# Kernel tuning notes

Hardware: AMD Instinct MI355X
Metric: run time of the kernel (lower is better)

The kernel has to match this reference:

```python
import jax, jax.numpy as jnp
import numpy as np

N, E, DIN, H, DOUT, NBLK = 50000, 300000, 963, 256, 3, 6


def gconv(x, src, dst, ew, W, Wl, b):
    # support = x @ W ; out[i] = sum_j ew_ij * support[j] + x[i] @ W_loop + b
    sup = x @ W
    agg = jax.ops.segment_sum(ew[:, None] * sup[src], dst, num_segments=N)
    return agg + x @ Wl + b


def setup_inputs() -> dict:
    key = jax.random.key(0)
    ks = jax.random.split(key, 16)
    s = 0.05
    x = jax.random.normal(ks[0], (N, DIN), jnp.float32)
    src = jax.random.randint(ks[1], (E,), 0, N, dtype=jnp.int32)
    dst = jax.random.randint(ks[2], (E,), 0, N, dtype=jnp.int32)
    ew = jax.random.uniform(ks[3], (E,), jnp.float32)
    W1 = jax.random.normal(ks[4], (DIN, H), jnp.float32) * s
    Wl1 = jax.random.normal(ks[5], (DIN, H), jnp.float32) * s
    b1 = jnp.zeros((H,), jnp.float32)
    # stacked residual-block weights: [NBLK, 2 convs, H, H]
    blkW = jax.random.normal(ks[6], (NBLK, 2, H, H), jnp.float32) * s
    blkWl = jax.random.normal(ks[7], (NBLK, 2, H, H), jnp.float32) * s
    blkb = jnp.zeros((NBLK, 2, H), jnp.float32)
    W2 = jax.random.normal(ks[8], (H, DOUT), jnp.float32) * s
    Wl2 = jax.random.normal(ks[9], (H, DOUT), jnp.float32) * s
    b2 = jnp.zeros((DOUT,), jnp.float32)
    return dict(x=x, src=src, dst=dst, ew=ew, W1=W1, Wl1=Wl1, b1=b1,
                blkW=blkW, blkWl=blkWl, blkb=blkb, W2=W2, Wl2=Wl2, b2=b2)


def reference(x, src, dst, ew, W1, Wl1, b1, blkW, blkWl, blkb, W2, Wl2, b2):
    h = jax.nn.relu(gconv(x, src, dst, ew, W1, Wl1, b1))

    def block(h, p):
        W, Wl, b = p  # W: [2,H,H]
        y = jax.nn.relu(gconv(h, src, dst, ew, W[0], Wl[0], b[0]))
        y = jax.nn.relu(gconv(y, src, dst, ew, W[1], Wl[1], b[1]))
        return (h + y) * 0.5, None

    x_hidden, _ = jax.lax.scan(block, h, (blkW, blkWl, blkb))
    x_out = gconv(x_hidden, src, dst, ew, W2, Wl2, b2)
    return (x_out, x_hidden)
```

## Files before the change

kernel.cpp:

```cpp
#include <hip/hip_runtime.h>

typedef __attribute__((ext_vector_type(8))) short short8;
typedef __attribute__((ext_vector_type(4))) float f32x4;

constexpr int kN = 50000;
constexpr int kE = 300000;
constexpr int kDIN = 963;
constexpr int kH = 256;
constexpr int kNBLK = 6;

__device__ inline unsigned short f2bf(float f) {
    unsigned u = __float_as_uint(f);
    u = u + 0x7FFFu + ((u >> 16) & 1u);
    return (unsigned short)(u >> 16);
}
__device__ inline float bf2f(unsigned short s) {
    return __uint_as_float(((unsigned)s) << 16);
}

__device__ inline void gload_lds16(const void* g, void* l) {
    __builtin_amdgcn_global_load_lds(
        (const __attribute__((address_space(1))) void*)g,
        (__attribute__((address_space(3))) void*)l, 16, 0, 0);
}

__global__ __launch_bounds__(512) void gemm_l1(
    const float* __restrict__ Av, const unsigned short* __restrict__ Bt,
    const float* __restrict__ bias,
    unsigned short* __restrict__ supb, unsigned short* __restrict__ tpreb,
    int M, int Kpad, int Kvalid, int Astride)
{
    __shared__ __align__(16) char smem[49152];
    char* As = smem;
    char* Bs = smem + 16384;

    const int tid = threadIdx.x;
    const int wid = tid >> 6;
    const int lane = tid & 63;
    const int wr = wid >> 2, wc = wid & 3;

    const int nwg = gridDim.x;
    const int q = nwg >> 3, r = nwg & 7;
    const int xcd = blockIdx.x & 7, idx = blockIdx.x >> 3;
    const int t = (xcd < r ? xcd * (q + 1) : r * (q + 1) + (xcd - r) * q) + idx;
    const int r0 = (t >> 1) * 128;
    const int c0 = (t & 1) * 256;

    f32x4 acc[4][4];
#pragma unroll
    for (int i = 0; i < 4; ++i)
#pragma unroll
        for (int j = 0; j < 4; ++j) acc[i][j] = f32x4{0.f, 0.f, 0.f, 0.f};

    const int l_row = lane >> 3;
    const int l_c   = lane & 7;

    for (int k0 = 0; k0 < Kpad; k0 += 64) {
#pragma unroll
        for (int p = 0; p < 4; ++p) {
            int row = wid * 32 + p * 8 + l_row;
            int csw = l_c ^ (row & 7);
            const unsigned short* g = Bt + (long)(c0 + row) * Kpad + k0 + csw * 8;
            gload_lds16(g, Bs + (wid * 32 + p * 8) * 128);
        }
        {
            const int row = tid >> 2;
            const int kq = tid & 3;
            int grow = r0 + row; if (grow >= M) grow = M - 1;
            const float* ar = Av + (long)grow * Astride;
#pragma unroll
            for (int j = 0; j < 2; ++j) {
                int k16 = kq * 2 + j;
                short8 v;
#pragma unroll
                for (int ii = 0; ii < 8; ++ii) {
                    int k = k0 + k16 * 8 + ii;
                    float f = (k < Kvalid) ? ar[k] : 0.f;
                    v[ii] = (short)f2bf(f);
                }
                *(short8*)(As + row * 128 + ((k16 ^ (row & 7)) << 4)) = v;
            }
        }
        __syncthreads();
#pragma unroll
        for (int kk = 0; kk < 2; ++kk) {
            short8 af[4], bfr[4];
            const int kg = kk * 4 + (lane >> 4);
#pragma unroll
            for (int nr = 0; nr < 4; ++nr) {
                int row = wr * 64 + nr * 16 + (lane & 15);
                af[nr] = *(const short8*)(As + row * 128 + ((kg ^ (row & 7)) << 4));
            }
#pragma unroll
            for (int mc = 0; mc < 4; ++mc) {
                int row = wc * 64 + mc * 16 + (lane & 15);
                bfr[mc] = *(const short8*)(Bs + row * 128 + ((kg ^ (row & 7)) << 4));
            }
#pragma unroll
            for (int mc = 0; mc < 4; ++mc)
#pragma unroll
                for (int nr = 0; nr < 4; ++nr)
                    acc[mc][nr] = __builtin_amdgcn_mfma_f32_16x16x32_bf16(
                        bfr[mc], af[nr], acc[mc][nr], 0, 0, 0);
        }
        __syncthreads();
    }

    const bool isSup = (c0 == 0);
    unsigned short* outp = isSup ? supb : tpreb;
    float* eL = (float*)smem;
    const int wrow = wr * 16 + (lane & 15);
    const int qc = (lane >> 4) << 2;

    for (int nr = 0; nr < 4; ++nr) {
        __syncthreads();
#pragma unroll
        for (int mc = 0; mc < 4; ++mc) {
            const int col = wc * 64 + mc * 16 + qc;
            f32x4 v = acc[mc][nr];
            if (!isSup) v += *(const f32x4*)(bias + col);
            const int c16 = col >> 2;
            *(f32x4*)(eL + wrow * 256 + ((c16 ^ wrow) << 2)) = v;
        }
        __syncthreads();
        const int tr = tid >> 4, j = tid & 15;
        const int gr = r0 + (tr >> 4) * 64 + nr * 16 + (tr & 15);
        if (gr < M) {
#pragma unroll
            for (int p = 0; p < 2; ++p) {
                const int u = j + 16 * p;
                f32x4 lo = *(const f32x4*)(eL + tr * 256 + (((2 * u) ^ tr) << 2));
                f32x4 hi = *(const f32x4*)(eL + tr * 256 + (((2 * u + 1) ^ tr) << 2));
                uint4 pk;
                pk.x = (unsigned)f2bf(lo[0]) | ((unsigned)f2bf(lo[1]) << 16);
                pk.y = (unsigned)f2bf(lo[2]) | ((unsigned)f2bf(lo[3]) << 16);
                pk.z = (unsigned)f2bf(hi[0]) | ((unsigned)f2bf(hi[1]) << 16);
                pk.w = (unsigned)f2bf(hi[2]) | ((unsigned)f2bf(hi[3]) << 16);
                *(uint4*)(outp + (long)gr * 256 + u * 8) = pk;
            }
        }
    }
}

template<int RES>
__global__ __launch_bounds__(512) void gemm_blk(
    const unsigned short* __restrict__ act, const unsigned short* __restrict__ xagg,
    const unsigned short* __restrict__ Bt, const float* __restrict__ bias,
    const unsigned short* __restrict__ hbf_res,
    unsigned short* __restrict__ outbf, float* __restrict__ hf32)
{
    __shared__ __align__(16) char smem[49152];
    char* As = smem;
    char* Bs = smem + 16384;

    const int tid = threadIdx.x;
    const int wid = tid >> 6;
    const int lane = tid & 63;
    const int wr = wid >> 2, wc = wid & 3;

    const int nwg = gridDim.x;
    const int q = nwg >> 3, r = nwg & 7;
    const int xcd = blockIdx.x & 7, idx = blockIdx.x >> 3;
    const int t = (xcd < r ? xcd * (q + 1) : r * (q + 1) + (xcd - r) * q) + idx;
    const int r0 = t * 128;

    f32x4 acc[4][4];
#pragma unroll
    for (int i = 0; i < 4; ++i)
#pragma unroll
        for (int j = 0; j < 4; ++j) acc[i][j] = f32x4{0.f, 0.f, 0.f, 0.f};

    const int l_row = lane >> 3;
    const int l_c   = lane & 7;

    for (int k0 = 0; k0 < 512; k0 += 64) {
#pragma unroll
        for (int p = 0; p < 4; ++p) {
            int row = wid * 32 + p * 8 + l_row;
            int csw = l_c ^ (row & 7);
            const unsigned short* g = Bt + (long)row * 512 + k0 + csw * 8;
            gload_lds16(g, Bs + (wid * 32 + p * 8) * 128);
        }
        const unsigned short* Asrc = (k0 < 256) ? (act + k0) : (xagg + (k0 - 256));
#pragma unroll
        for (int p = 0; p < 2; ++p) {
            int row = wid * 16 + p * 8 + l_row;
            int grow = r0 + row; if (grow >= kN) grow = kN - 1;
            int csw = l_c ^ (row & 7);
            const unsigned short* g = Asrc + (long)grow * 256 + csw * 8;
            gload_lds16(g, As + (wid * 16 + p * 8) * 128);
        }
        __syncthreads();
#pragma unroll
        for (int kk = 0; kk < 2; ++kk) {
            short8 af[4], bfr[4];
            const int kg = kk * 4 + (lane >> 4);
#pragma unroll
            for (int nr = 0; nr < 4; ++nr) {
                int row = wr * 64 + nr * 16 + (lane & 15);
                af[nr] = *(const short8*)(As + row * 128 + ((kg ^ (row & 7)) << 4));
            }
#pragma unroll
            for (int mc = 0; mc < 4; ++mc) {
                int row = wc * 64 + mc * 16 + (lane & 15);
                bfr[mc] = *(const short8*)(Bs + row * 128 + ((kg ^ (row & 7)) << 4));
            }
#pragma unroll
            for (int mc = 0; mc < 4; ++mc)
#pragma unroll
                for (int nr = 0; nr < 4; ++nr)
                    acc[mc][nr] = __builtin_amdgcn_mfma_f32_16x16x32_bf16(
                        bfr[mc], af[nr], acc[mc][nr], 0, 0, 0);
        }
        __syncthreads();
    }

    float* eL = (float*)smem;
    const int wrow = wr * 16 + (lane & 15);
    const int qc = (lane >> 4) << 2;

    for (int nr = 0; nr < 4; ++nr) {
        __syncthreads();
#pragma unroll
        for (int mc = 0; mc < 4; ++mc) {
            const int col = wc * 64 + mc * 16 + qc;
            f32x4 v = acc[mc][nr] + *(const f32x4*)(bias + col);
            const int c16 = col >> 2;
            *(f32x4*)(eL + wrow * 256 + ((c16 ^ wrow) << 2)) = v;
        }
        __syncthreads();
        const int tr = tid >> 4, j = tid & 15;
        const int gr = r0 + (tr >> 4) * 64 + nr * 16 + (tr & 15);
        if (gr < kN) {
#pragma unroll
            for (int p = 0; p < 2; ++p) {
                const int u = j + 16 * p;
                f32x4 lo = *(const f32x4*)(eL + tr * 256 + (((2 * u) ^ tr) << 2));
                f32x4 hi = *(const f32x4*)(eL + tr * 256 + (((2 * u + 1) ^ tr) << 2));
#pragma unroll
                for (int ii = 0; ii < 4; ++ii) {
                    lo[ii] = fmaxf(lo[ii], 0.f);
                    hi[ii] = fmaxf(hi[ii], 0.f);
                }
                if (RES >= 1) {
                    uint4 hv = *(const uint4*)(hbf_res + (long)gr * 256 + u * 8);
                    lo[0] = (bf2f((unsigned short)(hv.x & 0xFFFF)) + lo[0]) * 0.5f;
                    lo[1] = (bf2f((unsigned short)(hv.x >> 16))    + lo[1]) * 0.5f;
                    lo[2] = (bf2f((unsigned short)(hv.y & 0xFFFF)) + lo[2]) * 0.5f;
                    lo[3] = (bf2f((unsigned short)(hv.y >> 16))    + lo[3]) * 0.5f;
                    hi[0] = (bf2f((unsigned short)(hv.z & 0xFFFF)) + hi[0]) * 0.5f;
                    hi[1] = (bf2f((unsigned short)(hv.z >> 16))    + hi[1]) * 0.5f;
                    hi[2] = (bf2f((unsigned short)(hv.w & 0xFFFF)) + hi[2]) * 0.5f;
                    hi[3] = (bf2f((unsigned short)(hv.w >> 16))    + hi[3]) * 0.5f;
                }
                if (RES == 2) {
                    *(f32x4*)(hf32 + (long)gr * 256 + u * 8)     = lo;
                    *(f32x4*)(hf32 + (long)gr * 256 + u * 8 + 4) = hi;
                }
                uint4 pk;
                pk.x = (unsigned)f2bf(lo[0]) | ((unsigned)f2bf(lo[1]) << 16);
                pk.y = (unsigned)f2bf(lo[2]) | ((unsigned)f2bf(lo[3]) << 16);
                pk.z = (unsigned)f2bf(hi[0]) | ((unsigned)f2bf(hi[1]) << 16);
                pk.w = (unsigned)f2bf(hi[2]) | ((unsigned)f2bf(hi[3]) << 16);
                *(uint4*)(outbf + (long)gr * 256 + u * 8) = pk;
            }
        }
    }
}

__global__ __launch_bounds__(256) void agg0_kernel(
    const unsigned short* __restrict__ supb, const unsigned short* __restrict__ tpreb,
    const int* __restrict__ rowptr, const int* __restrict__ e_src,
    const float* __restrict__ e_w, unsigned short* __restrict__ obf)
{
    const int wid = threadIdx.x >> 6, lane = threadIdx.x & 63;
    const long node = (long)blockIdx.x * 4 + wid;
    if (node >= kN) return;
    const int c0 = lane << 2;

    ushort4 tv = *(const ushort4*)(tpreb + node * 256 + c0);
    f32x4 a = {bf2f(tv.x), bf2f(tv.y), bf2f(tv.z), bf2f(tv.w)};
    int b = rowptr[node];
    const int e = rowptr[node + 1];
    for (; b + 4 <= e; b += 4) {
        const int s0 = e_src[b],     s1 = e_src[b + 1];
        const int s2 = e_src[b + 2], s3 = e_src[b + 3];
        const float w0 = e_w[b],     w1 = e_w[b + 1];
        const float w2 = e_w[b + 2], w3 = e_w[b + 3];
        ushort4 v0 = *(const ushort4*)(supb + (long)s0 * 256 + c0);
        ushort4 v1 = *(const ushort4*)(supb + (long)s1 * 256 + c0);
        ushort4 v2 = *(const ushort4*)(supb + (long)s2 * 256 + c0);
        ushort4 v3 = *(const ushort4*)(supb + (long)s3 * 256 + c0);
        a[0] += w0 * bf2f(v0.x) + w1 * bf2f(v1.x) + w2 * bf2f(v2.x) + w3 * bf2f(v3.x);
        a[1] += w0 * bf2f(v0.y) + w1 * bf2f(v1.y) + w2 * bf2f(v2.y) + w3 * bf2f(v3.y);
        a[2] += w0 * bf2f(v0.z) + w1 * bf2f(v1.z) + w2 * bf2f(v2.z) + w3 * bf2f(v3.z);
        a[3] += w0 * bf2f(v0.w) + w1 * bf2f(v1.w) + w2 * bf2f(v2.w) + w3 * bf2f(v3.w);
    }
    for (; b < e; ++b) {
        const int s = e_src[b];
        const float w = e_w[b];
        ushort4 sv = *(const ushort4*)(supb + (long)s * 256 + c0);
        a[0] += w * bf2f(sv.x); a[1] += w * bf2f(sv.y);
        a[2] += w * bf2f(sv.z); a[3] += w * bf2f(sv.w);
    }
    uint2 pk;
    pk.x = (unsigned)f2bf(fmaxf(a[0], 0.f)) | ((unsigned)f2bf(fmaxf(a[1], 0.f)) << 16);
    pk.y = (unsigned)f2bf(fmaxf(a[2], 0.f)) | ((unsigned)f2bf(fmaxf(a[3], 0.f)) << 16);
    *(uint2*)(obf + node * 256 + c0) = pk;
}

__global__ __launch_bounds__(256) void aggx_kernel(
    const unsigned short* __restrict__ act,
    const int* __restrict__ rowptr, const int* __restrict__ e_src,
    const float* __restrict__ e_w, unsigned short* __restrict__ xagg)
{
    const int wid = threadIdx.x >> 6, lane = threadIdx.x & 63;
    const long node = (long)blockIdx.x * 4 + wid;
    if (node >= kN) return;
    const int c0 = lane << 2;

    f32x4 a = {0.f, 0.f, 0.f, 0.f};
    int b = rowptr[node];
    const int e = rowptr[node + 1];
    for (; b + 4 <= e; b += 4) {
        const int s0 = e_src[b],     s1 = e_src[b + 1];
        const int s2 = e_src[b + 2], s3 = e_src[b + 3];
        const float w0 = e_w[b],     w1 = e_w[b + 1];
        const float w2 = e_w[b + 2], w3 = e_w[b + 3];
        ushort4 v0 = *(const ushort4*)(act + (long)s0 * 256 + c0);
        ushort4 v1 = *(const ushort4*)(act + (long)s1 * 256 + c0);
        ushort4 v2 = *(const ushort4*)(act + (long)s2 * 256 + c0);
        ushort4 v3 = *(const ushort4*)(act + (long)s3 * 256 + c0);
        a[0] += w0 * bf2f(v0.x) + w1 * bf2f(v1.x) + w2 * bf2f(v2.x) + w3 * bf2f(v3.x);
        a[1] += w0 * bf2f(v0.y) + w1 * bf2f(v1.y) + w2 * bf2f(v2.y) + w3 * bf2f(v3.y);
        a[2] += w0 * bf2f(v0.z) + w1 * bf2f(v1.z) + w2 * bf2f(v2.z) + w3 * bf2f(v3.z);
        a[3] += w0 * bf2f(v0.w) + w1 * bf2f(v1.w) + w2 * bf2f(v2.w) + w3 * bf2f(v3.w);
    }
    for (; b < e; ++b) {
        const int s = e_src[b];
        const float w = e_w[b];
        ushort4 sv = *(const ushort4*)(act + (long)s * 256 + c0);
        a[0] += w * bf2f(sv.x); a[1] += w * bf2f(sv.y);
        a[2] += w * bf2f(sv.z); a[3] += w * bf2f(sv.w);
    }
    uint2 pk;
    pk.x = (unsigned)f2bf(a[0]) | ((unsigned)f2bf(a[1]) << 16);
    pk.y = (unsigned)f2bf(a[2]) | ((unsigned)f2bf(a[3]) << 16);
    *(uint2*)(xagg + node * 256 + c0) = pk;
}

__global__ __launch_bounds__(256) void cvt_w1_kernel(
    const float* __restrict__ W1, const float* __restrict__ Wl1,
    unsigned short* __restrict__ out)
{
    int idx = blockIdx.x * 256 + threadIdx.x;
    if (idx >= 512 * 1024) return;
    int c = idx >> 10, k = idx & 1023;
    float v = 0.f;
    if (k < kDIN) v = (c < 256) ? W1[(long)k * 256 + c] : Wl1[(long)k * 256 + (c - 256)];
    out[idx] = f2bf(v);
}

__global__ __launch_bounds__(256) void cvt_blk_kernel(
    const float* __restrict__ blkW, const float* __restrict__ blkWl,
    unsigned short* __restrict__ out)
{
    int idx = blockIdx.x * 256 + threadIdx.x;
    if (idx >= 12 * 256 * 512) return;
    int l = idx >> 17;
    int rem = idx & 131071;
    int c = rem >> 9, k = rem & 511;
    float v = (k < 256) ? blkWl[((long)l * 256 + k) * 256 + c]
                        : blkW[((long)l * 256 + (k - 256)) * 256 + c];
    out[idx] = f2bf(v);
}

__global__ __launch_bounds__(256) void hist_kernel(const int* __restrict__ dst,
                                                   int* __restrict__ counts)
{
    int e = blockIdx.x * 256 + threadIdx.x;
    if (e < kE) atomicAdd(&counts[dst[e]], 1);
}

__global__ __launch_bounds__(1024) void scan1_kernel(
    const int* __restrict__ counts, int* __restrict__ rowptr, int* __restrict__ bsum)
{
    __shared__ int s[1024];
    const int tid = threadIdx.x;
    const int g = blockIdx.x * 1024 + tid;
    const int v = (g < kN) ? counts[g] : 0;
    s[tid] = v; __syncthreads();
    for (int off = 1; off < 1024; off <<= 1) {
        int tv = (tid >= off) ? s[tid - off] : 0;
        __syncthreads();
        s[tid] += tv;
        __syncthreads();
    }
    if (g < kN) rowptr[g] = s[tid] - v;
    if (tid == 1023) bsum[blockIdx.x] = s[1023];
}

__global__ __launch_bounds__(64) void scan2_kernel(int* __restrict__ bsum, int nb)
{
    __shared__ int s[64];
    const int tid = threadIdx.x;
    const int v = (tid < nb) ? bsum[tid] : 0;
    s[tid] = v; __syncthreads();
    for (int off = 1; off < 64; off <<= 1) {
        int tv = (tid >= off) ? s[tid - off] : 0;
        __syncthreads();
        s[tid] += tv;
        __syncthreads();
    }
    if (tid < nb) bsum[tid] = s[tid] - v;
}

__global__ __launch_bounds__(256) void scan3_kernel(
    int* __restrict__ rowptr, const int* __restrict__ bsum, int* __restrict__ cursor)
{
    int g = blockIdx.x * 256 + threadIdx.x;
    if (g < kN) {
        int r = rowptr[g] + bsum[g >> 10];
        rowptr[g] = r;
        cursor[g] = r;
    }
    if (g == 0) rowptr[kN] = kE;
}

__global__ __launch_bounds__(256) void fill_kernel(
    const int* __restrict__ src, const int* __restrict__ dst,
    const float* __restrict__ ew, int* __restrict__ cursor,
    int* __restrict__ e_src, float* __restrict__ e_w)
{
    int e = blockIdx.x * 256 + threadIdx.x;
    if (e >= kE) return;
    int d = dst[e];
    int pos = atomicAdd(&cursor[d], 1);
    e_src[pos] = src[e];
    e_w[pos] = ew[e];
}

__global__ __launch_bounds__(64) void final_layer_kernel(
    const unsigned short* __restrict__ hbf, const float* __restrict__ W2,
    const float* __restrict__ Wl2, const float* __restrict__ b2,
    float* __restrict__ sup2, float* __restrict__ x_out)
{
    const int row = blockIdx.x;
    const int lane = threadIdx.x;
    const unsigned short* hr = hbf + (long)row * kH;
    float accW[3] = {0.f, 0.f, 0.f};
    float accL[3] = {0.f, 0.f, 0.f};
#pragma unroll
    for (int kb = 0; kb < kH / 64; ++kb) {
        int k = kb * 64 + lane;
        float v = bf2f(hr[k]);
#pragma unroll
        for (int c = 0; c < 3; ++c) {
            accW[c] = fmaf(v, W2[k * 3 + c], accW[c]);
            accL[c] = fmaf(v, Wl2[k * 3 + c], accL[c]);
        }
    }
#pragma unroll
    for (int off = 32; off > 0; off >>= 1) {
#pragma unroll
        for (int c = 0; c < 3; ++c) {
            accW[c] += __shfl_down(accW[c], off);
            accL[c] += __shfl_down(accL[c], off);
        }
    }
    if (lane == 0) {
#pragma unroll
        for (int c = 0; c < 3; ++c) {
            sup2[row * 3 + c] = accW[c];
            x_out[row * 3 + c] = accL[c] + b2[c];
        }
    }
}

__global__ __launch_bounds__(256) void scatter3_kernel(
    const float* __restrict__ sup2, const int* __restrict__ src,
    const int* __restrict__ dst, const float* __restrict__ ew,
    float* __restrict__ x_out)
{
    int e = blockIdx.x * 256 + threadIdx.x;
    if (e >= kE) return;
    int s = src[e];
    int d = dst[e];
    float w = ew[e];
#pragma unroll
    for (int c = 0; c < 3; ++c)
        atomicAdd(&x_out[(long)d * 3 + c], w * sup2[(long)s * 3 + c]);
}

extern "C" void kernel_launch(void* const* d_in, const int* in_sizes, int n_in,
                              void* d_out, int out_size, void* d_ws, size_t ws_size,
                              hipStream_t stream)
{
    const float* x    = (const float*)d_in[0];
    const int*   src  = (const int*)d_in[1];
    const int*   dst  = (const int*)d_in[2];
    const float* ew   = (const float*)d_in[3];
    const float* W1   = (const float*)d_in[4];
    const float* Wl1  = (const float*)d_in[5];
    const float* b1   = (const float*)d_in[6];
    const float* blkW  = (const float*)d_in[7];
    const float* blkWl = (const float*)d_in[8];
    const float* blkb  = (const float*)d_in[9];
    const float* W2   = (const float*)d_in[10];
    const float* Wl2  = (const float*)d_in[11];
    const float* b2   = (const float*)d_in[12];

    float* out   = (float*)d_out;
    float* x_out = out;
    float* h     = out + (long)kN * 3;

    char* w = (char*)d_ws;
    size_t off = 0;
    auto carve = [&](size_t bytes) { char* p = w + off; off = (off + bytes + 255) & ~(size_t)255; return p; };
    unsigned short* supb  = (unsigned short*)carve(12800000UL * 2);
    unsigned short* tpreb = (unsigned short*)carve(12800000UL * 2);
    unsigned short* tact  = (unsigned short*)carve(12800000UL * 2);
    unsigned short* hbf   = (unsigned short*)carve(12800000UL * 2);
    unsigned short* w1c   = (unsigned short*)carve(512UL * 1024 * 2);
    unsigned short* blkc  = (unsigned short*)carve(12UL * 256 * 512 * 2);
    int*   e_src  = (int*)carve(kE * 4);
    float* e_w    = (float*)carve(kE * 4);
    int*   counts = (int*)carve(50176 * 4);
    int*   rowptr = (int*)carve(50176 * 4);
    int*   cursor = (int*)carve(50176 * 4);
    int*   bsum   = (int*)carve(64 * 4);
    float* sup2   = (float*)carve((long)kN * 3 * 4);
    unsigned short* xagg = tpreb;

    hipMemsetAsync(counts, 0, 50176 * 4, stream);
    hist_kernel<<<(kE + 255) / 256, 256, 0, stream>>>(dst, counts);
    scan1_kernel<<<49, 1024, 0, stream>>>(counts, rowptr, bsum);
    scan2_kernel<<<1, 64, 0, stream>>>(bsum, 49);
    scan3_kernel<<<(kN + 255) / 256, 256, 0, stream>>>(rowptr, bsum, cursor);
    fill_kernel<<<(kE + 255) / 256, 256, 0, stream>>>(src, dst, ew, cursor, e_src, e_w);

    cvt_w1_kernel<<<2048, 256, 0, stream>>>(W1, Wl1, w1c);
    cvt_blk_kernel<<<6144, 256, 0, stream>>>(blkW, blkWl, blkc);

    const int l1_grid  = 2 * ((kN + 127) / 128);
    const int blk_grid = (kN + 127) / 128;
    const int agg_grid = (kN + 3) / 4;

    gemm_l1<<<l1_grid, 512, 0, stream>>>(x, w1c, b1, supb, tpreb,
                                         kN, 1024, kDIN, kDIN);
    agg0_kernel<<<agg_grid, 256, 0, stream>>>(supb, tpreb, rowptr, e_src, e_w, hbf);

    for (int l = 0; l < 2 * kNBLK; ++l) {
        const unsigned short* act_in = (l & 1) ? tact : hbf;
        unsigned short* act_out      = (l & 1) ? hbf : tact;
        aggx_kernel<<<agg_grid, 256, 0, stream>>>(act_in, rowptr, e_src, e_w, xagg);
        const unsigned short* B = blkc + (long)l * 256 * 512;
        const float* bb = blkb + (long)l * 256;
        if (l & 1) {
            if (l == 2 * kNBLK - 1)
                gemm_blk<2><<<blk_grid, 512, 0, stream>>>(act_in, xagg, B, bb, hbf, act_out, h);
            else
                gemm_blk<1><<<blk_grid, 512, 0, stream>>>(act_in, xagg, B, bb, hbf, act_out, nullptr);
        } else {
            gemm_blk<0><<<blk_grid, 512, 0, stream>>>(act_in, xagg, B, bb, nullptr, act_out, nullptr);
        }
    }

    final_layer_kernel<<<kN, 64, 0, stream>>>(hbf, W2, Wl2, b2, sup2, x_out);
    scatter3_kernel<<<(kE + 255) / 256, 256, 0, stream>>>(sup2, src, dst, ew, x_out);
}
```

Before: 1.020 ms.

## Split block GEMM into 128x128 tiles with 256 threads and vectorize layer-1 A loads

The residual-block GEMM now gives each workgroup a 128-row by 128-column output tile instead of 128 rows by all 256 columns. It uses 4 waves instead of 8, 32KB of LDS, and twice as many workgroups, which is meant to improve occupancy and load balance across CUs. The cost is that each A tile is loaded twice, once per column half. Separately, the layer-1 GEMM's fp32 A loads now use two unaligned float4 vector loads when all 8 elements are in range, replacing scalar loads with per-element bounds checks.

```diff
diff --git a/kernel.cpp b/kernel.cpp
--- a/kernel.cpp
+++ b/kernel.cpp
@@ -2,6 +2,7 @@
 
 typedef __attribute__((ext_vector_type(8))) short short8;
 typedef __attribute__((ext_vector_type(4))) float f32x4;
+typedef __attribute__((ext_vector_type(4), aligned(4))) float f32x4u;
 
 constexpr int kN = 50000;
 constexpr int kE = 300000;
@@ -71,12 +72,23 @@
 #pragma unroll
             for (int j = 0; j < 2; ++j) {
                 int k16 = kq * 2 + j;
+                int kb = k0 + k16 * 8;
                 short8 v;
-#pragma unroll
-                for (int ii = 0; ii < 8; ++ii) {
-                    int k = k0 + k16 * 8 + ii;
-                    float f = (k < Kvalid) ? ar[k] : 0.f;
-                    v[ii] = (short)f2bf(f);
+                if (kb + 8 <= Kvalid) {
+                    f32x4u f0 = *(const f32x4u*)(ar + kb);
+                    f32x4u f1 = *(const f32x4u*)(ar + kb + 4);
+#pragma unroll
+                    for (int ii = 0; ii < 4; ++ii) {
+                        v[ii]     = (short)f2bf(f0[ii]);
+                        v[ii + 4] = (short)f2bf(f1[ii]);
+                    }
+                } else {
+#pragma unroll
+                    for (int ii = 0; ii < 8; ++ii) {
+                        int k = kb + ii;
+                        float f = (k < Kvalid) ? ar[k] : 0.f;
+                        v[ii] = (short)f2bf(f);
+                    }
                 }
                 *(short8*)(As + row * 128 + ((k16 ^ (row & 7)) << 4)) = v;
             }
@@ -143,26 +155,27 @@
 }
 
 template<int RES>
-__global__ __launch_bounds__(512) void gemm_blk(
+__global__ __launch_bounds__(256) void gemm_blk(
     const unsigned short* __restrict__ act, const unsigned short* __restrict__ xagg,
     const unsigned short* __restrict__ Bt, const float* __restrict__ bias,
     const unsigned short* __restrict__ hbf_res,
     unsigned short* __restrict__ outbf, float* __restrict__ hf32)
 {
-    __shared__ __align__(16) char smem[49152];
+    __shared__ __align__(16) char smem[32768];
     char* As = smem;
     char* Bs = smem + 16384;
 
     const int tid = threadIdx.x;
     const int wid = tid >> 6;
     const int lane = tid & 63;
-    const int wr = wid >> 2, wc = wid & 3;
+    const int wr = wid >> 1, wc = wid & 1;
 
     const int nwg = gridDim.x;
     const int q = nwg >> 3, r = nwg & 7;
     const int xcd = blockIdx.x & 7, idx = blockIdx.x >> 3;
     const int t = (xcd < r ? xcd * (q + 1) : r * (q + 1) + (xcd - r) * q) + idx;
-    const int r0 = t * 128;
+    const int r0 = (t >> 1) * 128;
+    const int c0 = (t & 1) * 128;
 
     f32x4 acc[4][4];
 #pragma unroll
@@ -178,17 +191,17 @@
         for (int p = 0; p < 4; ++p) {
             int row = wid * 32 + p * 8 + l_row;
             int csw = l_c ^ (row & 7);
-            const unsigned short* g = Bt + (long)row * 512 + k0 + csw * 8;
+            const unsigned short* g = Bt + (long)(c0 + row) * 512 + k0 + csw * 8;
             gload_lds16(g, Bs + (wid * 32 + p * 8) * 128);
         }
         const unsigned short* Asrc = (k0 < 256) ? (act + k0) : (xagg + (k0 - 256));
 #pragma unroll
-        for (int p = 0; p < 2; ++p) {
-            int row = wid * 16 + p * 8 + l_row;
+        for (int p = 0; p < 4; ++p) {
+            int row = wid * 32 + p * 8 + l_row;
             int grow = r0 + row; if (grow >= kN) grow = kN - 1;
             int csw = l_c ^ (row & 7);
             const unsigned short* g = Asrc + (long)grow * 256 + csw * 8;
-            gload_lds16(g, As + (wid * 16 + p * 8) * 128);
+            gload_lds16(g, As + (wid * 32 + p * 8) * 128);
         }
         __syncthreads();
 #pragma unroll
@@ -224,26 +237,27 @@
 #pragma unroll
         for (int mc = 0; mc < 4; ++mc) {
             const int col = wc * 64 + mc * 16 + qc;
-            f32x4 v = acc[mc][nr] + *(const f32x4*)(bias + col);
+            f32x4 v = acc[mc][nr] + *(const f32x4*)(bias + c0 + col);
             const int c16 = col >> 2;
-            *(f32x4*)(eL + wrow * 256 + ((c16 ^ wrow) << 2)) = v;
-        }
-        __syncthreads();
-        const int tr = tid >> 4, j = tid & 15;
+            *(f32x4*)(eL + wrow * 128 + ((c16 ^ wrow) << 2)) = v;
+        }
+        __syncthreads();
+        const int tr = tid >> 3, j = tid & 7;
         const int gr = r0 + (tr >> 4) * 64 + nr * 16 + (tr & 15);
         if (gr < kN) {
 #pragma unroll
             for (int p = 0; p < 2; ++p) {
-                const int u = j + 16 * p;
-                f32x4 lo = *(const f32x4*)(eL + tr * 256 + (((2 * u) ^ tr) << 2));
-                f32x4 hi = *(const f32x4*)(eL + tr * 256 + (((2 * u + 1) ^ tr) << 2));
+                const int u = j + 8 * p;
+                f32x4 lo = *(const f32x4*)(eL + tr * 128 + (((2 * u) ^ tr) << 2));
+                f32x4 hi = *(const f32x4*)(eL + tr * 128 + (((2 * u + 1) ^ tr) << 2));
 #pragma unroll
                 for (int ii = 0; ii < 4; ++ii) {
                     lo[ii] = fmaxf(lo[ii], 0.f);
                     hi[ii] = fmaxf(hi[ii], 0.f);
                 }
+                const long gcol = (long)gr * 256 + c0 + u * 8;
                 if (RES >= 1) {
-                    uint4 hv = *(const uint4*)(hbf_res + (long)gr * 256 + u * 8);
+                    uint4 hv = *(const uint4*)(hbf_res + gcol);
                     lo[0] = (bf2f((unsigned short)(hv.x & 0xFFFF)) + lo[0]) * 0.5f;
                     lo[1] = (bf2f((unsigned short)(hv.x >> 16))    + lo[1]) * 0.5f;
                     lo[2] = (bf2f((unsigned short)(hv.y & 0xFFFF)) + lo[2]) * 0.5f;
@@ -254,15 +268,15 @@
                     hi[3] = (bf2f((unsigned short)(hv.w >> 16))    + hi[3]) * 0.5f;
                 }
                 if (RES == 2) {
-                    *(f32x4*)(hf32 + (long)gr * 256 + u * 8)     = lo;
-                    *(f32x4*)(hf32 + (long)gr * 256 + u * 8 + 4) = hi;
+                    *(f32x4*)(hf32 + gcol)     = lo;
+                    *(f32x4*)(hf32 + gcol + 4) = hi;
                 }
                 uint4 pk;
                 pk.x = (unsigned)f2bf(lo[0]) | ((unsigned)f2bf(lo[1]) << 16);
                 pk.y = (unsigned)f2bf(lo[2]) | ((unsigned)f2bf(lo[3]) << 16);
                 pk.z = (unsigned)f2bf(hi[0]) | ((unsigned)f2bf(hi[1]) << 16);
                 pk.w = (unsigned)f2bf(hi[2]) | ((unsigned)f2bf(hi[3]) << 16);
-                *(uint4*)(outbf + (long)gr * 256 + u * 8) = pk;
+                *(uint4*)(outbf + gcol) = pk;
             }
         }
     }
@@ -543,7 +557,7 @@
     cvt_blk_kernel<<<6144, 256, 0, stream>>>(blkW, blkWl, blkc);
 
     const int l1_grid  = 2 * ((kN + 127) / 128);
-    const int blk_grid = (kN + 127) / 128;
+    const int blk_grid = 2 * ((kN + 127) / 128);
     const int agg_grid = (kN + 3) / 4;
 
     gemm_l1<<<l1_grid, 512, 0, stream>>>(x, w1c, b1, supb, tpreb,
@@ -558,11 +572,11 @@
         const float* bb = blkb + (long)l * 256;
         if (l & 1) {
             if (l == 2 * kNBLK - 1)
-                gemm_blk<2><<<blk_grid, 512, 0, stream>>>(act_in, xagg, B, bb, hbf, act_out, h);
+                gemm_blk<2><<<blk_grid, 256, 0, stream>>>(act_in, xagg, B, bb, hbf, act_out, h);
             else
-                gemm_blk<1><<<blk_grid, 512, 0, stream>>>(act_in, xagg, B, bb, hbf, act_out, nullptr);
+                gemm_blk<1><<<blk_grid, 256, 0, stream>>>(act_in, xagg, B, bb, hbf, act_out, nullptr);
         } else {
-            gemm_blk<0><<<blk_grid, 512, 0, stream>>>(act_in, xagg, B, bb, nullptr, act_out, nullptr);
+            gemm_blk<0><<<blk_grid, 256, 0, stream>>>(act_in, xagg, B, bb, nullptr, act_out, nullptr);
         }
     }
 
```

Measured after the change: 979.4 us. -4.0%, faster.
